# Kernel optimization log

Measured on AMD Instinct MI355X. Metric: run time of the kernel, lower is better.

## Reference

```python
import jax, jax.numpy as jnp
import numpy as np

HIDDEN = 1024
FEAT = 2048
BOTTLENECK = 512
B, T = 64, 512


def setup_inputs() -> dict:
    key = jax.random.key(0)
    k1, k2, k3, k4, k5 = jax.random.split(key, 5)
    hidden = jax.random.normal(k1, (B, HIDDEN), dtype=jnp.float32)
    feats = jax.random.normal(k2, (B, T, FEAT), dtype=jnp.float32)
    # nn.Linear weights stored as [out, in]; apply as x @ W.T
    W = jax.random.normal(k3, (BOTTLENECK, HIDDEN), dtype=jnp.float32) * (1.0 / np.sqrt(HIDDEN))
    U = jax.random.normal(k4, (BOTTLENECK, FEAT), dtype=jnp.float32) * (1.0 / np.sqrt(FEAT))
    b = jnp.ones((BOTTLENECK,), dtype=jnp.float32)
    w = jax.random.normal(k5, (1, BOTTLENECK), dtype=jnp.float32) * (1.0 / np.sqrt(BOTTLENECK))
    return {"hidden": hidden, "feats": feats, "W": W, "U": U, "b": b, "w": w}


def reference(hidden, feats, W, U, b, w):
    Wh = hidden @ W.T                      # [B, K]
    Uv = jnp.einsum('btf,kf->btk', feats, U)  # [B, T, K]
    e = jnp.tanh(Wh[:, None, :] + Uv + b)  # [B, T, K]
    energies = jnp.einsum('btk,ok->bto', e, w)  # [B, T, 1]
    weights = jax.nn.softmax(energies, axis=1)  # softmax over time
    attn_feats = jnp.sum(feats * weights, axis=1)  # [B, F]
    return attn_feats, weights
```

## Files before the change

### kernel.cpp

```cpp
#include <hip/hip_runtime.h>
#include <hip/hip_bf16.h>
#include <math.h>

#define BATCH 64
#define TDIM 512
#define FEAT 2048
#define HID 1024
#define KDIM 512
#define MROWS (BATCH * TDIM)
#define TCH 16
#define TCLEN (TDIM / TCH)

typedef __attribute__((ext_vector_type(8))) short short8;
typedef __attribute__((ext_vector_type(4))) float floatx4;

#define GLL16(g, l)                                                     \
    __builtin_amdgcn_global_load_lds(                                   \
        (const __attribute__((address_space(1))) void*)(g),             \
        (__attribute__((address_space(3))) void*)(l), 16, 0, 0)

__device__ __forceinline__ unsigned short f2bf(float x) {
    unsigned int u = __float_as_uint(x);
    u += 0x7FFFu + ((u >> 16) & 1u);
    return (unsigned short)(u >> 16);
}

__global__ __launch_bounds__(256) void k_convert2(const float* __restrict__ feats,
                                                  const float* __restrict__ U,
                                                  unsigned short* __restrict__ fB,
                                                  unsigned short* __restrict__ uB,
                                                  int n4f, int n4tot) {
    int stride = gridDim.x * blockDim.x;
    for (int i = blockIdx.x * blockDim.x + threadIdx.x; i < n4tot; i += stride) {
        const float4* src = (i < n4f) ? (const float4*)feats + i
                                      : (const float4*)U + (i - n4f);
        ushort4* dst = (i < n4f) ? (ushort4*)fB + i
                                 : (ushort4*)uB + (i - n4f);
        float4 v = *src;
        ushort4 o;
        o.x = f2bf(v.x); o.y = f2bf(v.y); o.z = f2bf(v.z); o.w = f2bf(v.w);
        *dst = o;
    }
}

__global__ __launch_bounds__(256) void k1_whb(const float* __restrict__ hidden,
                                              const float* __restrict__ W,
                                              const float* __restrict__ bias,
                                              float* __restrict__ whb) {
    int b = blockIdx.y;
    int k = blockIdx.x * 4 + (threadIdx.x >> 6);
    int lane = threadIdx.x & 63;
    const float* hrow = hidden + (size_t)b * HID;
    const float* wrow = W + (size_t)k * HID;
    float acc = 0.f;
    #pragma unroll 4
    for (int h = lane; h < HID; h += 64) acc += hrow[h] * wrow[h];
    #pragma unroll
    for (int off = 32; off > 0; off >>= 1) acc += __shfl_down(acc, off, 64);
    if (lane == 0) whb[b * KDIM + k] = acc + bias[k];
}

__global__ __launch_bounds__(256, 2) void k2_mfma(const unsigned short* __restrict__ fB,
                                                  const unsigned short* __restrict__ uB,
                                                  const float* __restrict__ whb,
                                                  const float* __restrict__ wvec,
                                                  float* __restrict__ partial) {
    __shared__ unsigned short As[256 * 32];
    __shared__ unsigned short Bs[128 * 32];
    __shared__ float sums[2][256];

    const int tid  = threadIdx.x;
    const int wave = tid >> 6;
    const int lane = tid & 63;
    const int row0 = blockIdx.x * 256;
    const int k0   = blockIdx.y * 128;
    const int wm = wave >> 1, wn = wave & 1;
    const int col = lane & 15, quad = lane >> 4;

    const unsigned short* gA[4];
    unsigned short* lA[4];
    #pragma unroll
    for (int g = 0; g < 4; ++g) {
        int s = wave * 256 + g * 64 + lane;
        int r = s >> 2;
        int q = (s & 3) ^ ((r >> 1) & 3);
        gA[g] = fB + (size_t)(row0 + r) * FEAT + q * 8;
        lA[g] = As + (wave * 256 + g * 64) * 8;
    }
    const unsigned short* gBp[2];
    unsigned short* lB[2];
    #pragma unroll
    for (int g = 0; g < 2; ++g) {
        int s = wave * 128 + g * 64 + lane;
        int r = s >> 2;
        int q = (s & 3) ^ ((r >> 1) & 3);
        gBp[g] = uB + (size_t)(k0 + r) * FEAT + q * 8;
        lB[g] = Bs + (wave * 128 + g * 64) * 8;
    }

    const int sw = (quad ^ ((col >> 1) & 3)) * 8;

    floatx4 acc[8][4];
    #pragma unroll
    for (int i = 0; i < 8; ++i)
        #pragma unroll
        for (int j = 0; j < 4; ++j) acc[i][j] = (floatx4){0.f, 0.f, 0.f, 0.f};

    for (int f0 = 0; f0 < FEAT; f0 += 32) {
        #pragma unroll
        for (int g = 0; g < 4; ++g) { GLL16(gA[g], lA[g]); gA[g] += 32; }
        #pragma unroll
        for (int g = 0; g < 2; ++g) { GLL16(gBp[g], lB[g]); gBp[g] += 32; }
        __syncthreads();

        short8 af[8], bf[4];
        #pragma unroll
        for (int i = 0; i < 8; ++i)
            af[i] = *(const short8*)&As[(wm * 128 + i * 16 + col) * 32 + sw];
        #pragma unroll
        for (int j = 0; j < 4; ++j)
            bf[j] = *(const short8*)&Bs[(wn * 64 + j * 16 + col) * 32 + sw];
        #pragma unroll
        for (int i = 0; i < 8; ++i)
            #pragma unroll
            for (int j = 0; j < 4; ++j)
                acc[i][j] = __builtin_amdgcn_mfma_f32_16x16x32_bf16(
                    af[i], bf[j], acc[i][j], 0, 0, 0);
        __syncthreads();
    }

    const int b = row0 >> 9;
    float wk[4], hk[4];
    #pragma unroll
    for (int j = 0; j < 4; ++j) {
        int k = k0 + wn * 64 + j * 16 + col;
        wk[j] = wvec[k];
        hk[j] = whb[b * KDIM + k];
    }
    #pragma unroll
    for (int i = 0; i < 8; ++i) {
        #pragma unroll
        for (int r = 0; r < 4; ++r) {
            float s = 0.f;
            #pragma unroll
            for (int j = 0; j < 4; ++j)
                s += tanhf(acc[i][j][r] + hk[j]) * wk[j];
            #pragma unroll
            for (int off = 8; off > 0; off >>= 1)
                s += __shfl_down(s, off, 16);
            if (col == 0)
                sums[wn][wm * 128 + i * 16 + quad * 4 + r] = s;
        }
    }
    __syncthreads();
    partial[blockIdx.y * MROWS + row0 + tid] = sums[0][tid] + sums[1][tid];
}

#define BM 128
#define BN 128
#define BF 16
#define LDSPAD 4

__global__ __launch_bounds__(256) void k2_energy(const float* __restrict__ feats,
                                                 const float* __restrict__ U,
                                                 const float* __restrict__ whb,
                                                 const float* __restrict__ wvec,
                                                 float* __restrict__ partial) {
    __shared__ __align__(16) float As[BF][BM + LDSPAD];
    __shared__ __align__(16) float Us[BF][BN + LDSPAD];

    const int row0 = blockIdx.x * BM;
    const int k0   = blockIdx.y * BN;
    const int tid  = threadIdx.x;
    const int tx   = tid & 15;
    const int ty   = tid >> 4;

    float acc[8][8];
    #pragma unroll
    for (int i = 0; i < 8; ++i)
        #pragma unroll
        for (int j = 0; j < 8; ++j) acc[i][j] = 0.f;

    for (int f0 = 0; f0 < FEAT; f0 += BF) {
        #pragma unroll
        for (int l = 0; l < 2; ++l) {
            int li = tid + l * 256;
            int r  = li >> 2;
            int c4 = (li & 3) * 4;
            float4 av = *(const float4*)(feats + (size_t)(row0 + r) * FEAT + f0 + c4);
            float4 uv = *(const float4*)(U     + (size_t)(k0   + r) * FEAT + f0 + c4);
            As[c4 + 0][r] = av.x; As[c4 + 1][r] = av.y;
            As[c4 + 2][r] = av.z; As[c4 + 3][r] = av.w;
            Us[c4 + 0][r] = uv.x; Us[c4 + 1][r] = uv.y;
            Us[c4 + 2][r] = uv.z; Us[c4 + 3][r] = uv.w;
        }
        __syncthreads();
        #pragma unroll
        for (int kf = 0; kf < BF; ++kf) {
            float4 a0 = *(const float4*)&As[kf][ty * 8];
            float4 a1 = *(const float4*)&As[kf][ty * 8 + 4];
            float4 u0 = *(const float4*)&Us[kf][tx * 8];
            float4 u1 = *(const float4*)&Us[kf][tx * 8 + 4];
            float a[8] = {a0.x, a0.y, a0.z, a0.w, a1.x, a1.y, a1.z, a1.w};
            float u[8] = {u0.x, u0.y, u0.z, u0.w, u1.x, u1.y, u1.z, u1.w};
            #pragma unroll
            for (int i = 0; i < 8; ++i)
                #pragma unroll
                for (int j = 0; j < 8; ++j) acc[i][j] += a[i] * u[j];
        }
        __syncthreads();
    }

    const int b = row0 >> 9;
    float psum[8];
    #pragma unroll
    for (int i = 0; i < 8; ++i) {
        float s = 0.f;
        #pragma unroll
        for (int j = 0; j < 8; ++j) {
            int k = k0 + tx * 8 + j;
            s += tanhf(acc[i][j] + whb[b * KDIM + k]) * wvec[k];
        }
        psum[i] = s;
    }
    #pragma unroll
    for (int off = 8; off > 0; off >>= 1)
        #pragma unroll
        for (int i = 0; i < 8; ++i) psum[i] += __shfl_down(psum[i], off, 16);

    if (tx == 0) {
        int c = blockIdx.y;
        #pragma unroll
        for (int i = 0; i < 8; ++i)
            partial[c * MROWS + row0 + ty * 8 + i] = psum[i];
    }
}

__global__ __launch_bounds__(512) void k3_softmax(const float* __restrict__ partial,
                                                  float* __restrict__ wout) {
    int b = blockIdx.x;
    int t = threadIdx.x;
    float e = 0.f;
    #pragma unroll
    for (int c = 0; c < 4; ++c) e += partial[c * MROWS + b * TDIM + t];

    __shared__ float sm[512];
    sm[t] = e;
    __syncthreads();
    #pragma unroll
    for (int s = 256; s > 0; s >>= 1) {
        if (t < s) sm[t] = fmaxf(sm[t], sm[t + s]);
        __syncthreads();
    }
    float m = sm[0];
    __syncthreads();
    float ex = __expf(e - m);
    sm[t] = ex;
    __syncthreads();
    #pragma unroll
    for (int s = 256; s > 0; s >>= 1) {
        if (t < s) sm[t] += sm[t + s];
        __syncthreads();
    }
    float inv = 1.f / sm[0];
    wout[b * TDIM + t] = ex * inv;
}

__global__ __launch_bounds__(256) void k4_partial(const float* __restrict__ feats,
                                                  const float* __restrict__ weights,
                                                  float* __restrict__ partial4) {
    int b  = blockIdx.z;
    int t0 = blockIdx.y * TCLEN;
    int f4 = (blockIdx.x * 256 + threadIdx.x) * 4;
    __shared__ float wsm[TCLEN];
    if (threadIdx.x < TCLEN) wsm[threadIdx.x] = weights[b * TDIM + t0 + threadIdx.x];
    __syncthreads();

    const float* fp = feats + (size_t)b * TDIM * FEAT + (size_t)t0 * FEAT + f4;
    float ax = 0.f, ay = 0.f, az = 0.f, aw = 0.f;
    float bx = 0.f, by = 0.f, bz = 0.f, bw = 0.f;
    #pragma unroll 4
    for (int t = 0; t < TCLEN; t += 4) {
        float4 v0 = *(const float4*)(fp + (size_t)(t + 0) * FEAT);
        float4 v1 = *(const float4*)(fp + (size_t)(t + 1) * FEAT);
        float4 v2 = *(const float4*)(fp + (size_t)(t + 2) * FEAT);
        float4 v3 = *(const float4*)(fp + (size_t)(t + 3) * FEAT);
        float w0 = wsm[t], w1 = wsm[t + 1], w2 = wsm[t + 2], w3 = wsm[t + 3];
        ax += v0.x * w0; ay += v0.y * w0; az += v0.z * w0; aw += v0.w * w0;
        bx += v1.x * w1; by += v1.y * w1; bz += v1.z * w1; bw += v1.w * w1;
        ax += v2.x * w2; ay += v2.y * w2; az += v2.z * w2; aw += v2.w * w2;
        bx += v3.x * w3; by += v3.y * w3; bz += v3.z * w3; bw += v3.w * w3;
    }
    float4 o;
    o.x = ax + bx; o.y = ay + by; o.z = az + bz; o.w = aw + bw;
    *(float4*)(partial4 + ((size_t)blockIdx.y * BATCH + b) * FEAT + f4) = o;
}

__global__ __launch_bounds__(256) void k5_reduce(const float* __restrict__ partial4,
                                                 float* __restrict__ out) {
    int i4 = blockIdx.x * 256 + threadIdx.x;
    float4 s = ((const float4*)partial4)[i4];
    #pragma unroll
    for (int c = 1; c < TCH; ++c) {
        float4 v = ((const float4*)partial4)[(size_t)c * (BATCH * FEAT / 4) + i4];
        s.x += v.x; s.y += v.y; s.z += v.z; s.w += v.w;
    }
    ((float4*)out)[i4] = s;
}

__global__ __launch_bounds__(256) void k4_direct(const float* __restrict__ feats,
                                                 const float* __restrict__ weights,
                                                 float* __restrict__ out) {
    int b = blockIdx.y;
    int f4 = (blockIdx.x * 256 + threadIdx.x) * 4;
    __shared__ float wsm[TDIM];
    wsm[threadIdx.x]       = weights[b * TDIM + threadIdx.x];
    wsm[threadIdx.x + 256] = weights[b * TDIM + 256 + threadIdx.x];
    __syncthreads();

    const float* fp = feats + (size_t)b * TDIM * FEAT + f4;
    float ax = 0.f, ay = 0.f, az = 0.f, aw = 0.f;
    for (int t = 0; t < TDIM; ++t) {
        float4 v = *(const float4*)(fp + (size_t)t * FEAT);
        float w = wsm[t];
        ax += v.x * w; ay += v.y * w; az += v.z * w; aw += v.w * w;
    }
    float4 o = {ax, ay, az, aw};
    *(float4*)(out + (size_t)b * FEAT + f4) = o;
}

extern "C" void kernel_launch(void* const* d_in, const int* in_sizes, int n_in,
                              void* d_out, int out_size, void* d_ws, size_t ws_size,
                              hipStream_t stream) {
    const float* hidden = (const float*)d_in[0];
    const float* feats  = (const float*)d_in[1];
    const float* W      = (const float*)d_in[2];
    const float* U      = (const float*)d_in[3];
    const float* bias   = (const float*)d_in[4];
    const float* wvec   = (const float*)d_in[5];

    float* out         = (float*)d_out;
    float* attn_out    = out;
    float* weights_out = out + (size_t)BATCH * FEAT;
    float* whb         = weights_out;
    float* partial     = attn_out;

    const size_t featsN = (size_t)MROWS * FEAT;
    const size_t uN     = (size_t)KDIM * FEAT;
    const size_t bf16Bytes = (featsN + uN) * sizeof(unsigned short);
    const size_t poolBytes = (size_t)TCH * BATCH * FEAT * sizeof(float);
    const bool fast = ws_size >= bf16Bytes + poolBytes;

    k1_whb<<<dim3(KDIM / 4, BATCH), 256, 0, stream>>>(hidden, W, bias, whb);

    if (fast) {
        unsigned short* fBf = (unsigned short*)d_ws;
        unsigned short* uBf = fBf + featsN;
        float* pool4 = (float*)((char*)d_ws + bf16Bytes);
        k_convert2<<<1024, 256, 0, stream>>>(feats, U, fBf, uBf,
                                             (int)(featsN / 4),
                                             (int)((featsN + uN) / 4));
        k2_mfma<<<dim3(MROWS / 256, KDIM / 128), 256, 0, stream>>>(
            fBf, uBf, whb, wvec, partial);
        k3_softmax<<<dim3(BATCH), 512, 0, stream>>>(partial, weights_out);
        k4_partial<<<dim3(FEAT / 1024, TCH, BATCH), 256, 0, stream>>>(
            feats, weights_out, pool4);
        k5_reduce<<<dim3(BATCH * FEAT / 4 / 256), 256, 0, stream>>>(pool4, attn_out);
    } else {
        k2_energy<<<dim3(MROWS / 128, KDIM / 128), 256, 0, stream>>>(
            feats, U, whb, wvec, partial);
        k3_softmax<<<dim3(BATCH), 512, 0, stream>>>(partial, weights_out);
        k4_direct<<<dim3(FEAT / 1024, BATCH), 256, 0, stream>>>(
            feats, weights_out, attn_out);
    }
}
```

Measured before the change: 547.1 us.

## Fuse conversion with Wh GEMV, widen MFMA K-tile, pool from bf16 feats

The fp32-to-bf16 conversion of feats and U is fused with the hidden@W.T GEMV into one launch that splits work by block index, which removes a separate kernel. The MFMA energy kernel now stages 64 features per iteration with an 8-way XOR swizzle, halving the number of barrier pairs. The weighted pooling reads the bf16 copy of feats instead of fp32, halving its memory traffic but lowering the precision of the attended features. The k4 grid is also reshaped so each block covers a full feature row for one time chunk.

Result: faster. 500.0 us (-8.6%).

```diff
diff --git a/kernel.cpp b/kernel.cpp
--- a/kernel.cpp
+++ b/kernel.cpp
@@ -11,6 +11,9 @@
 #define TCH 16
 #define TCLEN (TDIM / TCH)
 
+#define FEATS4 (MROWS * FEAT / 4)
+#define U4 (KDIM * FEAT / 4)
+
 typedef __attribute__((ext_vector_type(8))) short short8;
 typedef __attribute__((ext_vector_type(4))) float floatx4;
 
@@ -25,22 +28,298 @@
     return (unsigned short)(u >> 16);
 }
 
-__global__ __launch_bounds__(256) void k_convert2(const float* __restrict__ feats,
-                                                  const float* __restrict__ U,
-                                                  unsigned short* __restrict__ fB,
-                                                  unsigned short* __restrict__ uB,
-                                                  int n4f, int n4tot) {
-    int stride = gridDim.x * blockDim.x;
-    for (int i = blockIdx.x * blockDim.x + threadIdx.x; i < n4tot; i += stride) {
-        const float4* src = (i < n4f) ? (const float4*)feats + i
-                                      : (const float4*)U + (i - n4f);
-        ushort4* dst = (i < n4f) ? (ushort4*)fB + i
-                                 : (ushort4*)uB + (i - n4f);
-        float4 v = *src;
-        ushort4 o;
-        o.x = f2bf(v.x); o.y = f2bf(v.y); o.z = f2bf(v.z); o.w = f2bf(v.w);
-        *dst = o;
-    }
+__device__ __forceinline__ float bf2f(unsigned short s) {
+    return __uint_as_float(((unsigned int)s) << 16);
+}
+
+__global__ __launch_bounds__(256) void k0_fused(const float* __restrict__ feats,
+                                                const float* __restrict__ U,
+                                                const float* __restrict__ hidden,
+                                                const float* __restrict__ W,
+                                                const float* __restrict__ bias,
+                                                unsigned short* __restrict__ fB,
+                                                unsigned short* __restrict__ uB,
+                                                float* __restrict__ whb) {
+    int bx = blockIdx.x;
+    if (bx < 1792) {
+        int stride = 1792 * 256;
+        for (int i = bx * 256 + threadIdx.x; i < FEATS4; i += stride) {
+            float4 v = ((const float4*)feats)[i];
+            ushort4 o;
+            o.x = f2bf(v.x); o.y = f2bf(v.y); o.z = f2bf(v.z); o.w = f2bf(v.w);
+            ((ushort4*)fB)[i] = o;
+        }
+    } else if (bx < 2048) {
+        int stride = 256 * 256;
+        for (int i = (bx - 1792) * 256 + threadIdx.x; i < U4; i += stride) {
+            float4 v = ((const float4*)U)[i];
+            ushort4 o;
+            o.x = f2bf(v.x); o.y = f2bf(v.y); o.z = f2bf(v.z); o.w = f2bf(v.w);
+            ((ushort4*)uB)[i] = o;
+        }
+    } else {
+        int bid = bx - 2048;
+        int b = bid >> 7;
+        int k = (bid & 127) * 4 + (threadIdx.x >> 6);
+        int lane = threadIdx.x & 63;
+        const float* hrow = hidden + (size_t)b * HID;
+        const float* wrow = W + (size_t)k * HID;
+        float acc = 0.f;
+        #pragma unroll 4
+        for (int h = lane; h < HID; h += 64) acc += hrow[h] * wrow[h];
+        #pragma unroll
+        for (int off = 32; off > 0; off >>= 1) acc += __shfl_down(acc, off, 64);
+        if (lane == 0) whb[b * KDIM + k] = acc + bias[k];
+    }
+}
+
+__global__ __launch_bounds__(256, 2) void k2_mfma(const unsigned short* __restrict__ fB,
+                                                  const unsigned short* __restrict__ uB,
+                                                  const float* __restrict__ whb,
+                                                  const float* __restrict__ wvec,
+                                                  float* __restrict__ partial) {
+    __shared__ unsigned short As[256 * 64];
+    __shared__ unsigned short Bs[128 * 64];
+    __shared__ float sums[2][256];
+
+    const int tid  = threadIdx.x;
+    const int wave = tid >> 6;
+    const int lane = tid & 63;
+    const int row0 = blockIdx.x * 256;
+    const int k0   = blockIdx.y * 128;
+    const int wm = wave >> 1, wn = wave & 1;
+    const int col = lane & 15, quad = lane >> 4;
+
+    const unsigned short* gA[8];
+    unsigned short* lA[8];
+    #pragma unroll
+    for (int g = 0; g < 8; ++g) {
+        int s = wave * 512 + g * 64 + lane;
+        int r = s >> 3;
+        int q = (s & 7) ^ (r & 7);
+        gA[g] = fB + (size_t)(row0 + r) * FEAT + q * 8;
+        lA[g] = As + (wave * 512 + g * 64) * 8;
+    }
+    const unsigned short* gBp[4];
+    unsigned short* lB[4];
+    #pragma unroll
+    for (int g = 0; g < 4; ++g) {
+        int s = wave * 256 + g * 64 + lane;
+        int r = s >> 3;
+        int q = (s & 7) ^ (r & 7);
+        gBp[g] = uB + (size_t)(k0 + r) * FEAT + q * 8;
+        lB[g] = Bs + (wave * 256 + g * 64) * 8;
+    }
+
+    floatx4 acc[8][4];
+    #pragma unroll
+    for (int i = 0; i < 8; ++i)
+        #pragma unroll
+        for (int j = 0; j < 4; ++j) acc[i][j] = (floatx4){0.f, 0.f, 0.f, 0.f};
+
+    for (int f0 = 0; f0 < FEAT; f0 += 64) {
+        #pragma unroll
+        for (int g = 0; g < 8; ++g) { GLL16(gA[g], lA[g]); gA[g] += 64; }
+        #pragma unroll
+        for (int g = 0; g < 4; ++g) { GLL16(gBp[g], lB[g]); gBp[g] += 64; }
+        __syncthreads();
+
+        #pragma unroll
+        for (int kk = 0; kk < 2; ++kk) {
+            const int sw = ((kk * 4 + quad) ^ (col & 7)) * 8;
+            short8 af[8], bf[4];
+            #pragma unroll
+            for (int i = 0; i < 8; ++i)
+                af[i] = *(const short8*)&As[(wm * 128 + i * 16 + col) * 64 + sw];
+            #pragma unroll
+            for (int j = 0; j < 4; ++j)
+                bf[j] = *(const short8*)&Bs[(wn * 64 + j * 16 + col) * 64 + sw];
+            #pragma unroll
+            for (int i = 0; i < 8; ++i)
+                #pragma unroll
+                for (int j = 0; j < 4; ++j)
+                    acc[i][j] = __builtin_amdgcn_mfma_f32_16x16x32_bf16(
+                        af[i], bf[j], acc[i][j], 0, 0, 0);
+        }
+        __syncthreads();
+    }
+
+    const int b = row0 >> 9;
+    float wk[4], hk[4];
+    #pragma unroll
+    for (int j = 0; j < 4; ++j) {
+        int k = k0 + wn * 64 + j * 16 + col;
+        wk[j] = wvec[k];
+        hk[j] = whb[b * KDIM + k];
+    }
+    #pragma unroll
+    for (int i = 0; i < 8; ++i) {
+        #pragma unroll
+        for (int r = 0; r < 4; ++r) {
+            float s = 0.f;
+            #pragma unroll
+            for (int j = 0; j < 4; ++j)
+                s += tanhf(acc[i][j][r] + hk[j]) * wk[j];
+            #pragma unroll
+            for (int off = 8; off > 0; off >>= 1)
+                s += __shfl_down(s, off, 16);
+            if (col == 0)
+                sums[wn][wm * 128 + i * 16 + quad * 4 + r] = s;
+        }
+    }
+    __syncthreads();
+    partial[blockIdx.y * MROWS + row0 + tid] = sums[0][tid] + sums[1][tid];
+}
+
+#define BM 128
+#define BN 128
+#define BF 16
+#define LDSPAD 4
+
+__global__ __launch_bounds__(256) void k2_energy(const float* __restrict__ feats,
+                                                 const float* __restrict__ U,
+                                                 const float* __restrict__ whb,
+                                                 const float* __restrict__ wvec,
+                                                 float* __restrict__ partial) {
+    __shared__ __align__(16) float As[BF][BM + LDSPAD];
+    __shared__ __align__(16) float Us[BF][BN + LDSPAD];
+
+    const int row0 = blockIdx.x * BM;
+    const int k0   = blockIdx.y * BN;
+    const int tid  = threadIdx.x;
+    const int tx   = tid & 15;
+    const int ty   = tid >> 4;
+
+    float acc[8][8];
+    #pragma unroll
+    for (int i = 0; i < 8; ++i)
+        #pragma unroll
+        for (int j = 0; j < 8; ++j) acc[i][j] = 0.f;
+
+    for (int f0 = 0; f0 < FEAT; f0 += BF) {
+        #pragma unroll
+        for (int l = 0; l < 2; ++l) {
+            int li = tid + l * 256;
+            int r  = li >> 2;
+            int c4 = (li & 3) * 4;
+            float4 av = *(const float4*)(feats + (size_t)(row0 + r) * FEAT + f0 + c4);
+            float4 uv = *(const float4*)(U     + (size_t)(k0   + r) * FEAT + f0 + c4);
+            As[c4 + 0][r] = av.x; As[c4 + 1][r] = av.y;
+            As[c4 + 2][r] = av.z; As[c4 + 3][r] = av.w;
+            Us[c4 + 0][r] = uv.x; Us[c4 + 1][r] = uv.y;
+            Us[c4 + 2][r] = uv.z; Us[c4 + 3][r] = uv.w;
+        }
+        __syncthreads();
+        #pragma unroll
+        for (int kf = 0; kf < BF; ++kf) {
+            float4 a0 = *(const float4*)&As[kf][ty * 8];
+            float4 a1 = *(const float4*)&As[kf][ty * 8 + 4];
+            float4 u0 = *(const float4*)&Us[kf][tx * 8];
+            float4 u1 = *(const float4*)&Us[kf][tx * 8 + 4];
+            float a[8] = {a0.x, a0.y, a0.z, a0.w, a1.x, a1.y, a1.z, a1.w};
+            float u[8] = {u0.x, u0.y, u0.z, u0.w, u1.x, u1.y, u1.z, u1.w};
+            #pragma unroll
+            for (int i = 0; i < 8; ++i)
+                #pragma unroll
+                for (int j = 0; j < 8; ++j) acc[i][j] += a[i] * u[j];
+        }
+        __syncthreads();
+    }
+
+    const int b = row0 >> 9;
+    float psum[8];
+    #pragma unroll
+    for (int i = 0; i < 8; ++i) {
+        float s = 0.f;
+        #pragma unroll
+        for (int j = 0; j < 8; ++j) {
+            int k = k0 + tx * 8 + j;
+            s += tanhf(acc[i][j] + whb[b * KDIM + k]) * wvec[k];
+        }
+        psum[i] = s;
+    }
+    #pragma unroll
+    for (int off = 8; off > 0; off >>= 1)
+        #pragma unroll
+        for (int i = 0; i < 8; ++i) psum[i] += __shfl_down(psum[i], off, 16);
+
+    if (tx == 0) {
+        int c = blockIdx.y;
+        #pragma unroll
+        for (int i = 0; i < 8; ++i)
+            partial[c * MROWS + row0 + ty * 8 + i] = psum[i];
+    }
+}
+
+__global__ __launch_bounds__(512) void k3_softmax(const float* __restrict__ partial,
+                                                  float* __restrict__ wout) {
+    int b = blockIdx.x;
+    int t = threadIdx.x;
+    float e = 0.f;
+    #pragma unroll
+    for (int c = 0; c < 4; ++c) e += partial[c * MROWS + b * TDIM + t];
+
+    __shared__ float sm[512];
+    sm[t] = e;
+    __syncthreads();
+    #pragma unroll
+    for (int s = 256; s > 0; s >>= 1) {
+        if (t < s) sm[t] = fmaxf(sm[t], sm[t + s]);
+        __syncthreads();
+    }
+    float m = sm[0];
+    __syncthreads();
+    float ex = __expf(e - m);
+    sm[t] = ex;
+    __syncthreads();
+    #pragma unroll
+    for (int s = 256; s > 0; s >>= 1) {
+        if (t < s) sm[t] += sm[t + s];
+        __syncthreads();
+    }
+    float inv = 1.f / sm[0];
+    wout[b * TDIM + t] = ex * inv;
+}
+
+__global__ __launch_bounds__(256) void k4_partial_bf(const unsigned short* __restrict__ fB,
+                                                     const float* __restrict__ weights,
+                                                     float* __restrict__ partial4) {
+    int b  = blockIdx.y;
+    int t0 = blockIdx.x * TCLEN;
+    int f8 = threadIdx.x * 8;
+    __shared__ float wsm[TCLEN];
+    if (threadIdx.x < TCLEN) wsm[threadIdx.x] = weights[b * TDIM + t0 + threadIdx.x];
+    __syncthreads();
+
+    const unsigned short* fp = fB + ((size_t)b * TDIM + t0) * FEAT + f8;
+    float a[8];
+    #pragma unroll
+    for (int e = 0; e < 8; ++e) a[e] = 0.f;
+    #pragma unroll 4
+    for (int t = 0; t < TCLEN; ++t) {
+        short8 v = *(const short8*)(fp + (size_t)t * FEAT);
+        float w = wsm[t];
+        #pragma unroll
+        for (int e = 0; e < 8; ++e)
+            a[e] += bf2f((unsigned short)v[e]) * w;
+    }
+    float* op = partial4 + ((size_t)blockIdx.x * BATCH + b) * FEAT + f8;
+    float4 o0 = {a[0], a[1], a[2], a[3]};
+    float4 o1 = {a[4], a[5], a[6], a[7]};
+    *(float4*)op = o0;
+    *(float4*)(op + 4) = o1;
+}
+
+__global__ __launch_bounds__(256) void k5_reduce(const float* __restrict__ partial4,
+                                                 float* __restrict__ out) {
+    int i4 = blockIdx.x * 256 + threadIdx.x;
+    float4 s = ((const float4*)partial4)[i4];
+    #pragma unroll
+    for (int c = 1; c < TCH; ++c) {
+        float4 v = ((const float4*)partial4)[(size_t)c * (BATCH * FEAT / 4) + i4];
+        s.x += v.x; s.y += v.y; s.z += v.z; s.w += v.w;
+    }
+    ((float4*)out)[i4] = s;
 }
 
 __global__ __launch_bounds__(256) void k1_whb(const float* __restrict__ hidden,
@@ -60,254 +339,6 @@
     if (lane == 0) whb[b * KDIM + k] = acc + bias[k];
 }
 
-__global__ __launch_bounds__(256, 2) void k2_mfma(const unsigned short* __restrict__ fB,
-                                                  const unsigned short* __restrict__ uB,
-                                                  const float* __restrict__ whb,
-                                                  const float* __restrict__ wvec,
-                                                  float* __restrict__ partial) {
-    __shared__ unsigned short As[256 * 32];
-    __shared__ unsigned short Bs[128 * 32];
-    __shared__ float sums[2][256];
-
-    const int tid  = threadIdx.x;
-    const int wave = tid >> 6;
-    const int lane = tid & 63;
-    const int row0 = blockIdx.x * 256;
-    const int k0   = blockIdx.y * 128;
-    const int wm = wave >> 1, wn = wave & 1;
-    const int col = lane & 15, quad = lane >> 4;
-
-    const unsigned short* gA[4];
-    unsigned short* lA[4];
-    #pragma unroll
-    for (int g = 0; g < 4; ++g) {
-        int s = wave * 256 + g * 64 + lane;
-        int r = s >> 2;
-        int q = (s & 3) ^ ((r >> 1) & 3);
-        gA[g] = fB + (size_t)(row0 + r) * FEAT + q * 8;
-        lA[g] = As + (wave * 256 + g * 64) * 8;
-    }
-    const unsigned short* gBp[2];
-    unsigned short* lB[2];
-    #pragma unroll
-    for (int g = 0; g < 2; ++g) {
-        int s = wave * 128 + g * 64 + lane;
-        int r = s >> 2;
-        int q = (s & 3) ^ ((r >> 1) & 3);
-        gBp[g] = uB + (size_t)(k0 + r) * FEAT + q * 8;
-        lB[g] = Bs + (wave * 128 + g * 64) * 8;
-    }
-
-    const int sw = (quad ^ ((col >> 1) & 3)) * 8;
-
-    floatx4 acc[8][4];
-    #pragma unroll
-    for (int i = 0; i < 8; ++i)
-        #pragma unroll
-        for (int j = 0; j < 4; ++j) acc[i][j] = (floatx4){0.f, 0.f, 0.f, 0.f};
-
-    for (int f0 = 0; f0 < FEAT; f0 += 32) {
-        #pragma unroll
-        for (int g = 0; g < 4; ++g) { GLL16(gA[g], lA[g]); gA[g] += 32; }
-        #pragma unroll
-        for (int g = 0; g < 2; ++g) { GLL16(gBp[g], lB[g]); gBp[g] += 32; }
-        __syncthreads();
-
-        short8 af[8], bf[4];
-        #pragma unroll
-        for (int i = 0; i < 8; ++i)
-            af[i] = *(const short8*)&As[(wm * 128 + i * 16 + col) * 32 + sw];
-        #pragma unroll
-        for (int j = 0; j < 4; ++j)
-            bf[j] = *(const short8*)&Bs[(wn * 64 + j * 16 + col) * 32 + sw];
-        #pragma unroll
-        for (int i = 0; i < 8; ++i)
-            #pragma unroll
-            for (int j = 0; j < 4; ++j)
-                acc[i][j] = __builtin_amdgcn_mfma_f32_16x16x32_bf16(
-                    af[i], bf[j], acc[i][j], 0, 0, 0);
-        __syncthreads();
-    }
-
-    const int b = row0 >> 9;
-    float wk[4], hk[4];
-    #pragma unroll
-    for (int j = 0; j < 4; ++j) {
-        int k = k0 + wn * 64 + j * 16 + col;
-        wk[j] = wvec[k];
-        hk[j] = whb[b * KDIM + k];
-    }
-    #pragma unroll
-    for (int i = 0; i < 8; ++i) {
-        #pragma unroll
-        for (int r = 0; r < 4; ++r) {
-            float s = 0.f;
-            #pragma unroll
-            for (int j = 0; j < 4; ++j)
-                s += tanhf(acc[i][j][r] + hk[j]) * wk[j];
-            #pragma unroll
-            for (int off = 8; off > 0; off >>= 1)
-                s += __shfl_down(s, off, 16);
-            if (col == 0)
-                sums[wn][wm * 128 + i * 16 + quad * 4 + r] = s;
-        }
-    }
-    __syncthreads();
-    partial[blockIdx.y * MROWS + row0 + tid] = sums[0][tid] + sums[1][tid];
-}
-
-#define BM 128
-#define BN 128
-#define BF 16
-#define LDSPAD 4
-
-__global__ __launch_bounds__(256) void k2_energy(const float* __restrict__ feats,
-                                                 const float* __restrict__ U,
-                                                 const float* __restrict__ whb,
-                                                 const float* __restrict__ wvec,
-                                                 float* __restrict__ partial) {
-    __shared__ __align__(16) float As[BF][BM + LDSPAD];
-    __shared__ __align__(16) float Us[BF][BN + LDSPAD];
-
-    const int row0 = blockIdx.x * BM;
-    const int k0   = blockIdx.y * BN;
-    const int tid  = threadIdx.x;
-    const int tx   = tid & 15;
-    const int ty   = tid >> 4;
-
-    float acc[8][8];
-    #pragma unroll
-    for (int i = 0; i < 8; ++i)
-        #pragma unroll
-        for (int j = 0; j < 8; ++j) acc[i][j] = 0.f;
-
-    for (int f0 = 0; f0 < FEAT; f0 += BF) {
-        #pragma unroll
-        for (int l = 0; l < 2; ++l) {
-            int li = tid + l * 256;
-            int r  = li >> 2;
-            int c4 = (li & 3) * 4;
-            float4 av = *(const float4*)(feats + (size_t)(row0 + r) * FEAT + f0 + c4);
-            float4 uv = *(const float4*)(U     + (size_t)(k0   + r) * FEAT + f0 + c4);
-            As[c4 + 0][r] = av.x; As[c4 + 1][r] = av.y;
-            As[c4 + 2][r] = av.z; As[c4 + 3][r] = av.w;
-            Us[c4 + 0][r] = uv.x; Us[c4 + 1][r] = uv.y;
-            Us[c4 + 2][r] = uv.z; Us[c4 + 3][r] = uv.w;
-        }
-        __syncthreads();
-        #pragma unroll
-        for (int kf = 0; kf < BF; ++kf) {
-            float4 a0 = *(const float4*)&As[kf][ty * 8];
-            float4 a1 = *(const float4*)&As[kf][ty * 8 + 4];
-            float4 u0 = *(const float4*)&Us[kf][tx * 8];
-            float4 u1 = *(const float4*)&Us[kf][tx * 8 + 4];
-            float a[8] = {a0.x, a0.y, a0.z, a0.w, a1.x, a1.y, a1.z, a1.w};
-            float u[8] = {u0.x, u0.y, u0.z, u0.w, u1.x, u1.y, u1.z, u1.w};
-            #pragma unroll
-            for (int i = 0; i < 8; ++i)
-                #pragma unroll
-                for (int j = 0; j < 8; ++j) acc[i][j] += a[i] * u[j];
-        }
-        __syncthreads();
-    }
-
-    const int b = row0 >> 9;
-    float psum[8];
-    #pragma unroll
-    for (int i = 0; i < 8; ++i) {
-        float s = 0.f;
-        #pragma unroll
-        for (int j = 0; j < 8; ++j) {
-            int k = k0 + tx * 8 + j;
-            s += tanhf(acc[i][j] + whb[b * KDIM + k]) * wvec[k];
-        }
-        psum[i] = s;
-    }
-    #pragma unroll
-    for (int off = 8; off > 0; off >>= 1)
-        #pragma unroll
-        for (int i = 0; i < 8; ++i) psum[i] += __shfl_down(psum[i], off, 16);
-
-    if (tx == 0) {
-        int c = blockIdx.y;
-        #pragma unroll
-        for (int i = 0; i < 8; ++i)
-            partial[c * MROWS + row0 + ty * 8 + i] = psum[i];
-    }
-}
-
-__global__ __launch_bounds__(512) void k3_softmax(const float* __restrict__ partial,
-                                                  float* __restrict__ wout) {
-    int b = blockIdx.x;
-    int t = threadIdx.x;
-    float e = 0.f;
-    #pragma unroll
-    for (int c = 0; c < 4; ++c) e += partial[c * MROWS + b * TDIM + t];
-
-    __shared__ float sm[512];
-    sm[t] = e;
-    __syncthreads();
-    #pragma unroll
-    for (int s = 256; s > 0; s >>= 1) {
-        if (t < s) sm[t] = fmaxf(sm[t], sm[t + s]);
-        __syncthreads();
-    }
-    float m = sm[0];
-    __syncthreads();
-    float ex = __expf(e - m);
-    sm[t] = ex;
-    __syncthreads();
-    #pragma unroll
-    for (int s = 256; s > 0; s >>= 1) {
-        if (t < s) sm[t] += sm[t + s];
-        __syncthreads();
-    }
-    float inv = 1.f / sm[0];
-    wout[b * TDIM + t] = ex * inv;
-}
-
-__global__ __launch_bounds__(256) void k4_partial(const float* __restrict__ feats,
-                                                  const float* __restrict__ weights,
-                                                  float* __restrict__ partial4) {
-    int b  = blockIdx.z;
-    int t0 = blockIdx.y * TCLEN;
-    int f4 = (blockIdx.x * 256 + threadIdx.x) * 4;
-    __shared__ float wsm[TCLEN];
-    if (threadIdx.x < TCLEN) wsm[threadIdx.x] = weights[b * TDIM + t0 + threadIdx.x];
-    __syncthreads();
-
-    const float* fp = feats + (size_t)b * TDIM * FEAT + (size_t)t0 * FEAT + f4;
-    float ax = 0.f, ay = 0.f, az = 0.f, aw = 0.f;
-    float bx = 0.f, by = 0.f, bz = 0.f, bw = 0.f;
-    #pragma unroll 4
-    for (int t = 0; t < TCLEN; t += 4) {
-        float4 v0 = *(const float4*)(fp + (size_t)(t + 0) * FEAT);
-        float4 v1 = *(const float4*)(fp + (size_t)(t + 1) * FEAT);
-        float4 v2 = *(const float4*)(fp + (size_t)(t + 2) * FEAT);
-        float4 v3 = *(const float4*)(fp + (size_t)(t + 3) * FEAT);
-        float w0 = wsm[t], w1 = wsm[t + 1], w2 = wsm[t + 2], w3 = wsm[t + 3];
-        ax += v0.x * w0; ay += v0.y * w0; az += v0.z * w0; aw += v0.w * w0;
-        bx += v1.x * w1; by += v1.y * w1; bz += v1.z * w1; bw += v1.w * w1;
-        ax += v2.x * w2; ay += v2.y * w2; az += v2.z * w2; aw += v2.w * w2;
-        bx += v3.x * w3; by += v3.y * w3; bz += v3.z * w3; bw += v3.w * w3;
-    }
-    float4 o;
-    o.x = ax + bx; o.y = ay + by; o.z = az + bz; o.w = aw + bw;
-    *(float4*)(partial4 + ((size_t)blockIdx.y * BATCH + b) * FEAT + f4) = o;
-}
-
-__global__ __launch_bounds__(256) void k5_reduce(const float* __restrict__ partial4,
-                                                 float* __restrict__ out) {
-    int i4 = blockIdx.x * 256 + threadIdx.x;
-    float4 s = ((const float4*)partial4)[i4];
-    #pragma unroll
-    for (int c = 1; c < TCH; ++c) {
-        float4 v = ((const float4*)partial4)[(size_t)c * (BATCH * FEAT / 4) + i4];
-        s.x += v.x; s.y += v.y; s.z += v.z; s.w += v.w;
-    }
-    ((float4*)out)[i4] = s;
-}
-
 __global__ __launch_bounds__(256) void k4_direct(const float* __restrict__ feats,
                                                  const float* __restrict__ weights,
                                                  float* __restrict__ out) {
@@ -351,22 +382,20 @@
     const size_t poolBytes = (size_t)TCH * BATCH * FEAT * sizeof(float);
     const bool fast = ws_size >= bf16Bytes + poolBytes;
 
-    k1_whb<<<dim3(KDIM / 4, BATCH), 256, 0, stream>>>(hidden, W, bias, whb);
-
     if (fast) {
         unsigned short* fBf = (unsigned short*)d_ws;
         unsigned short* uBf = fBf + featsN;
         float* pool4 = (float*)((char*)d_ws + bf16Bytes);
-        k_convert2<<<1024, 256, 0, stream>>>(feats, U, fBf, uBf,
-                                             (int)(featsN / 4),
-                                             (int)((featsN + uN) / 4));
+        k0_fused<<<dim3(10240), 256, 0, stream>>>(feats, U, hidden, W, bias,
+                                                  fBf, uBf, whb);
         k2_mfma<<<dim3(MROWS / 256, KDIM / 128), 256, 0, stream>>>(
             fBf, uBf, whb, wvec, partial);
         k3_softmax<<<dim3(BATCH), 512, 0, stream>>>(partial, weights_out);
-        k4_partial<<<dim3(FEAT / 1024, TCH, BATCH), 256, 0, stream>>>(
-            feats, weights_out, pool4);
+        k4_partial_bf<<<dim3(TCH, BATCH), 256, 0, stream>>>(
+            fBf, weights_out, pool4);
         k5_reduce<<<dim3(BATCH * FEAT / 4 / 256), 256, 0, stream>>>(pool4, attn_out);
     } else {
+        k1_whb<<<dim3(KDIM / 4, BATCH), 256, 0, stream>>>(hidden, W, bias, whb);
         k2_energy<<<dim3(MROWS / 128, KDIM / 128), 256, 0, stream>>>(
             feats, U, whb, wvec, partial);
         k3_softmax<<<dim3(BATCH), 512, 0, stream>>>(partial, weights_out);
```
